# Kernel optimization log

Measured on AMD Instinct MI355X. Metric: run time of the kernel, lower is better.

The kernel has to match this reference:

```python
import jax, jax.numpy as jnp
import numpy as np

K = 3
STRIDE = 1
PAD = 1
DIL = 1


def _unfold(a):
    # a: (N, C, H, W) -> patches (N, C, K*K, oH, oW), matching torch.F.unfold
    # channel-major ordering (c slowest, then kernel row, then kernel col).
    N, C, H, W = a.shape
    oH = (H + 2 * PAD - DIL * (K - 1) - 1) // STRIDE + 1
    oW = (W + 2 * PAD - DIL * (K - 1) - 1) // STRIDE + 1
    ap = jnp.pad(a, ((0, 0), (0, 0), (PAD, PAD), (PAD, PAD)))
    cols = []
    for i in range(K):
        for j in range(K):
            cols.append(ap[:, :,
                           i * DIL: i * DIL + (oH - 1) * STRIDE + 1: STRIDE,
                           j * DIL: j * DIL + (oW - 1) * STRIDE + 1: STRIDE])
    return jnp.stack(cols, axis=2)  # (N, C, K*K, oH, oW)


def setup_inputs() -> dict:
    key = jax.random.key(0)
    k1, k2, k3, k4, k5 = jax.random.split(key, 5)
    N, C, O, H, W = 4, 128, 256, 128, 128
    x = jax.random.normal(k1, (N, C, H, W), dtype=jnp.float32)
    depth = jax.random.uniform(k2, (N, 1, H, W), dtype=jnp.float32)
    camera_params = jax.random.normal(k3, (N, 4), dtype=jnp.float32)
    weight = jax.random.normal(k4, (O, C, K, K), dtype=jnp.float32) * 0.05
    bias = jax.random.normal(k5, (O,), dtype=jnp.float32) * 0.05
    return {"x": x, "depth": depth, "camera_params": camera_params,
            "weight": weight, "bias": bias}


def reference(x, depth, camera_params, weight, bias):
    # camera_params is accepted but unused, mirroring the torch module.
    O, C = weight.shape[0], weight.shape[1]
    xp = _unfold(x)        # (N, C, kk, oH, oW)
    dp = _unfold(depth)    # (N, 1, kk, oH, oW)
    w = weight.reshape(O, C, K * K)
    # depth-modulated im2col GEMM: sum_{c,p} w[o,c,p] * x_patch * d_patch
    out = jnp.einsum('ocp,ncpxy->noxy', w, xp * dp)
    return out + bias[None, :, None, None]
```

## Files before the change

kernel.cpp:

```cpp
#include <hip/hip_runtime.h>
#include <stdint.h>


#define C_IN 128
#define O_OUT 256
#define HW 128
#define NB 4
#define PADW 130

#define XD_ELEMS ((size_t)NB * PADW * PADW * C_IN)
#define XD_BYTES (XD_ELEMS * 2)
#define WT_ELEMS ((size_t)O_OUT * C_IN * 9)
#define WT_BYTES (WT_ELEMS * 2)

typedef __attribute__((ext_vector_type(8))) short short8;
typedef __attribute__((ext_vector_type(4))) float f32x4;
typedef __attribute__((ext_vector_type(2))) float f32x2;
typedef __attribute__((ext_vector_type(4))) unsigned uint4v;

__device__ __forceinline__ unsigned f2bf_bits(float f) {
  unsigned u = __builtin_bit_cast(unsigned, f);
  return (u + 0x7fffu + ((u >> 16) & 1u)) >> 16;
}

__device__ __forceinline__ void async_load16(const void* g, void* l) {
  __builtin_amdgcn_global_load_lds(
      (__attribute__((address_space(1))) void*)g,
      (__attribute__((address_space(3))) void*)l, 16, 0, 0);
}

__global__ __launch_bounds__(256) void prep_all(const float* __restrict__ x,
                                                const float* __restrict__ depth,
                                                const float* __restrict__ w,
                                                short* __restrict__ xd,
                                                short* __restrict__ wt2) {
  const int R = blockIdx.x;
  const int tid = threadIdx.x;

  if (R >= NB * HW * 2 + NB) {
    int gid = (R - (NB * HW * 2 + NB)) * 4608 + tid;
#pragma unroll
    for (int i = 0; i < 18; ++i, gid += 256) {
      const int j = gid & 7;
      const int lane = (gid >> 3) & 63;
      const int t = (gid >> 9) & 3;
      const int wm = (gid >> 11) & 1;
      const int g2 = gid >> 12;
      const int s = g2 % 36;
      const int o0 = g2 / 36;
      const int ln = lane & 15, q = lane >> 4;
      const int o = (o0 << 7) + (wm << 6) + (t << 4) + ln;
      const int cc = s / 9;
      const int tap = s % 9;
      const int c = (cc << 5) + (q << 3) + j;
      wt2[gid] = (short)f2bf_bits(w[((size_t)o * C_IN + c) * 9 + tap]);
    }
    return;
  }

  if (R >= NB * HW * 2) {
    const int n = R - NB * HW * 2;
    uint4v* base0 = (uint4v*)(xd + (size_t)n * PADW * PADW * C_IN);
    uint4v* base1 = (uint4v*)(xd + ((size_t)n * PADW + (PADW - 1)) * PADW * C_IN);
    const uint4v z = {0u, 0u, 0u, 0u};
    const int per_row = PADW * C_IN * 2 / 16;
    for (int i = tid; i < per_row; i += 256) {
      base0[i] = z;
      base1[i] = z;
    }
    return;
  }

  __shared__ __align__(16) unsigned s32[HW * 36];

  const int n = R >> 8;
  const int y = (R >> 1) & 127;
  const int h = R & 1;
  const int lane = tid & 63;
  const int wave = tid >> 6;

  {
    unsigned* row = (unsigned*)(xd + (size_t)(n * PADW + y + 1) * PADW * C_IN);
    if (tid < 32) row[(h << 5) + tid] = 0u;
    else if (tid < 64) row[(size_t)(PADW - 1) * 64 + (h << 5) + (tid - 32)] = 0u;
  }

  const f32x2 d2 = *(const f32x2*)(depth + ((size_t)n * HW + y) * HW + 2 * lane);
  const float* xrow =
      x + (((size_t)(n * C_IN + (h << 6)) * HW) + y) * HW + 2 * lane;
#pragma unroll
  for (int it = 0; it < 8; ++it) {
    const int cp = (wave << 3) + it;
    const f32x2 va = *(const f32x2*)(xrow + (size_t)(2 * cp) * HW * HW);
    const f32x2 vb = *(const f32x2*)(xrow + (size_t)(2 * cp + 1) * HW * HW);
    s32[(2 * lane) * 36 + cp] =
        f2bf_bits(va.x * d2.x) | (f2bf_bits(vb.x * d2.x) << 16);
    s32[(2 * lane + 1) * 36 + cp] =
        f2bf_bits(va.y * d2.y) | (f2bf_bits(vb.y * d2.y) << 16);
  }
  __syncthreads();

  unsigned* orow = (unsigned*)(xd + ((size_t)(n * PADW + y + 1) * PADW + 1) * C_IN);
#pragma unroll
  for (int i = 0; i < 4; ++i) {
    const int flat = tid + (i << 8);
    const int px = flat >> 3, jj = flat & 7;
    const uint4v v = *(const uint4v*)&s32[px * 36 + (jj << 2)];
    *(uint4v*)&orow[(size_t)px * 64 + (h << 5) + (jj << 2)] = v;
  }
}

__global__ __launch_bounds__(256, 2) void conv_mfma(
    const short* __restrict__ xd, const short* __restrict__ wt2,
    const float* __restrict__ bias, float* __restrict__ out) {
  __shared__ __align__(16) short xbuf[2][16640];

  const int tid = threadIdx.x;
  const int bx = blockIdx.x;
  const int n = bx >> 6;
  const int y = (bx & 63) << 1;
  const int o0b = blockIdx.y;
  const int lane = tid & 63;
  const int wave = tid >> 6;
  const int wm = wave & 1, wn = wave >> 1;
  const int ln = lane & 15, q = lane >> 4;

  const short* wbase = wt2 + (size_t)o0b * 147456 + (wm << 11) + (lane << 3);

  const short* xsrc0 = xd + (size_t)(n * PADW + y) * PADW * C_IN +
                       (tid >> 2) * C_IN + (tid & 3) * 8;

  f32x4 acc[4][8] = {};
  short8 areg[2][4];

  auto loadA = [&](int s, int p) {
#pragma unroll
    for (int t = 0; t < 4; ++t)
      areg[p][t] = *(const short8*)(wbase + (size_t)s * 4096 + t * 512);
  };

  {
    short* xdst = &xbuf[0][0] + tid * 8;
#pragma unroll
    for (int j = 0; j < 8; ++j)
      async_load16(xsrc0 + j * 8192, xdst + j * 2048);
    if (tid < 32) async_load16(xsrc0 + 8 * 8192, xdst + 8 * 2048);
  }
  loadA(0, 0);
  __syncthreads();

#pragma unroll
  for (int cc = 0; cc < 4; ++cc) {
#pragma unroll
    for (int tap = 0; tap < 9; ++tap) {
      const int s = cc * 9 + tap;
      if (s + 1 < 36) loadA(s + 1, (s + 1) & 1);

      if (cc + 1 < 4) {
        const short* sp = xsrc0 + ((cc + 1) << 5);
        short* xdst = &xbuf[(cc + 1) & 1][0] + tid * 8;
        if (tap < 8) async_load16(sp + tap * 8192, xdst + tap * 2048);
        if (tap == 0 && tid < 32)
          async_load16(sp + 8 * 8192, xdst + 8 * 2048);
      }

      const int ti = tap / 3, tj = tap % 3;
      const int rbase = (wn + ti) * 130 + tj;

      short8 b[8];
#pragma unroll
      for (int u = 0; u < 8; ++u)
        b[u] = *(const short8*)(&xbuf[cc & 1][0] +
                                (rbase + (u << 4) + ln) * 32 + (q << 3));
      __builtin_amdgcn_s_setprio(1);
#pragma unroll
      for (int t = 0; t < 4; ++t)
#pragma unroll
        for (int u = 0; u < 8; ++u)
          acc[t][u] = __builtin_amdgcn_mfma_f32_16x16x32_bf16(
              areg[s & 1][t], b[u], acc[t][u], 0, 0, 0);
      __builtin_amdgcn_s_setprio(0);
    }
    if (cc + 1 < 4) __syncthreads();
  }

#pragma unroll
  for (int t = 0; t < 4; ++t) {
    const int ob = (o0b << 7) + (wm << 6) + (t << 4) + (q << 2);
#pragma unroll
    for (int u = 0; u < 8; ++u) {
      const int xcol = (u << 4) + ln;
      const int yrow = y + wn;
#pragma unroll
      for (int r = 0; r < 4; ++r) {
        const int o = ob + r;
        out[(((size_t)n * O_OUT + o) * HW + yrow) * HW + xcol] =
            acc[t][u][r] + bias[o];
      }
    }
  }
}

__global__ void conv_naive(const float* __restrict__ x,
                           const float* __restrict__ depth,
                           const float* __restrict__ w,
                           const float* __restrict__ bias,
                           float* __restrict__ out) {
  const int gid = blockIdx.x * 256 + threadIdx.x;
  if (gid >= NB * O_OUT * HW * HW) return;
  const int xc = gid & 127;
  const int y = (gid >> 7) & 127;
  const int o = (gid >> 14) & 255;
  const int n = gid >> 22;
  float s = bias[o];
  for (int c = 0; c < C_IN; ++c)
    for (int i = 0; i < 3; ++i) {
      const int yy = y + i - 1;
      if (yy < 0 || yy >= HW) continue;
      for (int j = 0; j < 3; ++j) {
        const int xx = xc + j - 1;
        if (xx < 0 || xx >= HW) continue;
        s += w[((o * C_IN + c) * 3 + i) * 3 + j] *
             x[(((size_t)n * C_IN + c) * HW + yy) * HW + xx] *
             depth[((size_t)n * HW + yy) * HW + xx];
      }
    }
  out[gid] = s;
}

extern "C" void kernel_launch(void* const* d_in, const int* in_sizes, int n_in,
                              void* d_out, int out_size, void* d_ws, size_t ws_size,
                              hipStream_t stream) {
  const float* x = (const float*)d_in[0];
  const float* depth = (const float*)d_in[1];
  const float* weight = (const float*)d_in[3];
  const float* bias = (const float*)d_in[4];
  float* out = (float*)d_out;

  const size_t need = XD_BYTES + WT_BYTES;
  if (ws_size < need) {
    conv_naive<<<(NB * O_OUT * HW * HW + 255) / 256, 256, 0, stream>>>(
        x, depth, weight, bias, out);
    return;
  }

  short* xd = (short*)d_ws;
  short* wt2 = (short*)((char*)d_ws + XD_BYTES);

  prep_all<<<NB * HW * 2 + NB + 64, 256, 0, stream>>>(x, depth, weight, xd, wt2);
  conv_mfma<<<dim3(NB * HW / 2, 2), 256, 0, stream>>>(xd, wt2, bias, out);
}
```

Before: 128.4 us.

## Retile conv waves to cover all 128 outputs and half the pixel columns

Each wave in the MFMA conv kernel now computes 128 output channels by 64 pixels instead of 64 channels by 128 pixels. Every wave loads 8 weight fragments from global per step and only 4 activation fragments from LDS, which cuts LDS reads but doubles global/L2 weight traffic per wave and the areg register footprint. The weight prep layout is rewritten to match, and the activation prep now does per-lane scalar loads packed into 16-byte LDS stores instead of 2-wide loads with scattered 4-byte stores. The larger weight register set may put pressure on occupancy at the two-blocks-per-CU launch bound.

```diff
diff --git a/kernel.cpp b/kernel.cpp
--- a/kernel.cpp
+++ b/kernel.cpp
@@ -43,13 +43,12 @@
     for (int i = 0; i < 18; ++i, gid += 256) {
       const int j = gid & 7;
       const int lane = (gid >> 3) & 63;
-      const int t = (gid >> 9) & 3;
-      const int wm = (gid >> 11) & 1;
+      const int T = (gid >> 9) & 7;
       const int g2 = gid >> 12;
       const int s = g2 % 36;
       const int o0 = g2 / 36;
       const int ln = lane & 15, q = lane >> 4;
-      const int o = (o0 << 7) + (wm << 6) + (t << 4) + ln;
+      const int o = (o0 << 7) + (T << 4) + ln;
       const int cc = s / 9;
       const int tap = s % 9;
       const int c = (cc << 5) + (q << 3) + j;
@@ -85,18 +84,26 @@
     else if (tid < 64) row[(size_t)(PADW - 1) * 64 + (h << 5) + (tid - 32)] = 0u;
   }
 
-  const f32x2 d2 = *(const f32x2*)(depth + ((size_t)n * HW + y) * HW + 2 * lane);
-  const float* xrow =
-      x + (((size_t)(n * C_IN + (h << 6)) * HW) + y) * HW + 2 * lane;
-#pragma unroll
-  for (int it = 0; it < 8; ++it) {
-    const int cp = (wave << 3) + it;
-    const f32x2 va = *(const f32x2*)(xrow + (size_t)(2 * cp) * HW * HW);
-    const f32x2 vb = *(const f32x2*)(xrow + (size_t)(2 * cp + 1) * HW * HW);
-    s32[(2 * lane) * 36 + cp] =
-        f2bf_bits(va.x * d2.x) | (f2bf_bits(vb.x * d2.x) << 16);
-    s32[(2 * lane + 1) * 36 + cp] =
-        f2bf_bits(va.y * d2.y) | (f2bf_bits(vb.y * d2.y) << 16);
+  const float d0 = depth[((size_t)n * HW + y) * HW + lane];
+  const float d1 = depth[((size_t)n * HW + y) * HW + 64 + lane];
+  const float* xbase = x + (((size_t)(n * C_IN + (h << 6)) * HW) + y) * HW;
+#pragma unroll
+  for (int gg = 0; gg < 2; ++gg) {
+    const int g = (wave << 1) + gg;
+    const float* xc = xbase + ((size_t)(g << 3)) * HW * HW;
+#pragma unroll
+    for (int ph = 0; ph < 2; ++ph) {
+      const int px = (ph << 6) + lane;
+      const float d = ph ? d1 : d0;
+      uint4v v;
+#pragma unroll
+      for (int k = 0; k < 4; ++k) {
+        const float a = xc[(size_t)(2 * k) * HW * HW + px];
+        const float b2 = xc[(size_t)(2 * k + 1) * HW * HW + px];
+        v[k] = f2bf_bits(a * d) | (f2bf_bits(b2 * d) << 16);
+      }
+      *(uint4v*)&s32[px * 36 + (g << 2)] = v;
+    }
   }
   __syncthreads();
 
@@ -122,20 +129,21 @@
   const int o0b = blockIdx.y;
   const int lane = tid & 63;
   const int wave = tid >> 6;
-  const int wm = wave & 1, wn = wave >> 1;
+  const int wn = wave & 1;
+  const int wp = wave >> 1;
   const int ln = lane & 15, q = lane >> 4;
 
-  const short* wbase = wt2 + (size_t)o0b * 147456 + (wm << 11) + (lane << 3);
+  const short* wbase = wt2 + (size_t)o0b * 147456 + (lane << 3);
 
   const short* xsrc0 = xd + (size_t)(n * PADW + y) * PADW * C_IN +
                        (tid >> 2) * C_IN + (tid & 3) * 8;
 
-  f32x4 acc[4][8] = {};
-  short8 areg[2][4];
+  f32x4 acc[8][4] = {};
+  short8 areg[2][8];
 
   auto loadA = [&](int s, int p) {
 #pragma unroll
-    for (int t = 0; t < 4; ++t)
+    for (int t = 0; t < 8; ++t)
       areg[p][t] = *(const short8*)(wbase + (size_t)s * 4096 + t * 512);
   };
 
@@ -165,18 +173,18 @@
       }
 
       const int ti = tap / 3, tj = tap % 3;
-      const int rbase = (wn + ti) * 130 + tj;
-
-      short8 b[8];
-#pragma unroll
-      for (int u = 0; u < 8; ++u)
+      const int rbase = (wn + ti) * 130 + tj + (wp << 6);
+
+      short8 b[4];
+#pragma unroll
+      for (int u = 0; u < 4; ++u)
         b[u] = *(const short8*)(&xbuf[cc & 1][0] +
                                 (rbase + (u << 4) + ln) * 32 + (q << 3));
       __builtin_amdgcn_s_setprio(1);
 #pragma unroll
-      for (int t = 0; t < 4; ++t)
-#pragma unroll
-        for (int u = 0; u < 8; ++u)
+      for (int t = 0; t < 8; ++t)
+#pragma unroll
+        for (int u = 0; u < 4; ++u)
           acc[t][u] = __builtin_amdgcn_mfma_f32_16x16x32_bf16(
               areg[s & 1][t], b[u], acc[t][u], 0, 0, 0);
       __builtin_amdgcn_s_setprio(0);
@@ -184,13 +192,13 @@
     if (cc + 1 < 4) __syncthreads();
   }
 
-#pragma unroll
-  for (int t = 0; t < 4; ++t) {
-    const int ob = (o0b << 7) + (wm << 6) + (t << 4) + (q << 2);
-#pragma unroll
-    for (int u = 0; u < 8; ++u) {
-      const int xcol = (u << 4) + ln;
-      const int yrow = y + wn;
+  const int yrow = y + wn;
+#pragma unroll
+  for (int t = 0; t < 8; ++t) {
+    const int ob = (o0b << 7) + (t << 4) + (q << 2);
+#pragma unroll
+    for (int u = 0; u < 4; ++u) {
+      const int xcol = (wp << 6) + (u << 4) + ln;
 #pragma unroll
       for (int r = 0; r < 4; ++r) {
         const int o = ob + r;
```

Result: slower. 137.6 us (+7.2%).

## Prefetch B fragments into registers, XOR-swizzle LDS layout, remap block order

Applied to the files above, without the earlier changes.

The B operand is now double-buffered in registers, so each tap reads the next tap's fragments from LDS while the MFMAs for the current tap run. The 16-byte chunks within each pixel's 32-channel LDS slot are XOR-swizzled to cut bank conflicts on the strided reads. The 2D grid is flattened into a swizzled 1D block index that interleaves output-channel halves and spreads row blocks across XCDs to improve L2 locality. The extra breg array raises register pressure, which may hurt occupancy under launch_bounds(256,2).

```diff
diff --git a/kernel.cpp b/kernel.cpp
--- a/kernel.cpp
+++ b/kernel.cpp
@@ -116,10 +116,11 @@
   __shared__ __align__(16) short xbuf[2][16640];
 
   const int tid = threadIdx.x;
-  const int bx = blockIdx.x;
+  const int swz = ((blockIdx.x & 7) << 6) + (blockIdx.x >> 3);
+  const int o0b = swz & 1;
+  const int bx = swz >> 1;
   const int n = bx >> 6;
   const int y = (bx & 63) << 1;
-  const int o0b = blockIdx.y;
   const int lane = tid & 63;
   const int wave = tid >> 6;
   const int wm = wave & 1, wn = wave >> 1;
@@ -128,16 +129,26 @@
   const short* wbase = wt2 + (size_t)o0b * 147456 + (wm << 11) + (lane << 3);
 
   const short* xsrc0 = xd + (size_t)(n * PADW + y) * PADW * C_IN +
-                       (tid >> 2) * C_IN + (tid & 3) * 8;
+                       (tid >> 2) * C_IN + ((tid & 3) ^ ((tid >> 3) & 3)) * 8;
 
   f32x4 acc[4][8] = {};
   short8 areg[2][4];
+  short8 breg[2][8];
 
   auto loadA = [&](int s, int p) {
 #pragma unroll
     for (int t = 0; t < 4; ++t)
       areg[p][t] = *(const short8*)(wbase + (size_t)s * 4096 + t * 512);
   };
+  auto readB = [&](int buf, int ti, int tj, int p) {
+    const int rbase = (wn + ti) * 130 + tj;
+#pragma unroll
+    for (int u = 0; u < 8; ++u) {
+      const int px = rbase + (u << 4) + ln;
+      const int qx = (q ^ ((px >> 1) & 3)) << 3;
+      breg[p][u] = *(const short8*)(&xbuf[buf][0] + px * 32 + qx);
+    }
+  };
 
   {
     short* xdst = &xbuf[0][0] + tid * 8;
@@ -148,6 +159,7 @@
   }
   loadA(0, 0);
   __syncthreads();
+  readB(0, 0, 0, 0);
 
 #pragma unroll
   for (int cc = 0; cc < 4; ++cc) {
@@ -164,33 +176,30 @@
           async_load16(sp + 8 * 8192, xdst + 8 * 2048);
       }
 
-      const int ti = tap / 3, tj = tap % 3;
-      const int rbase = (wn + ti) * 130 + tj;
-
-      short8 b[8];
-#pragma unroll
-      for (int u = 0; u < 8; ++u)
-        b[u] = *(const short8*)(&xbuf[cc & 1][0] +
-                                (rbase + (u << 4) + ln) * 32 + (q << 3));
+      if (tap < 8) readB(cc & 1, (tap + 1) / 3, (tap + 1) % 3, (tap + 1) & 1);
+
       __builtin_amdgcn_s_setprio(1);
 #pragma unroll
       for (int t = 0; t < 4; ++t)
 #pragma unroll
         for (int u = 0; u < 8; ++u)
           acc[t][u] = __builtin_amdgcn_mfma_f32_16x16x32_bf16(
-              areg[s & 1][t], b[u], acc[t][u], 0, 0, 0);
+              areg[s & 1][t], breg[tap & 1][u], acc[t][u], 0, 0, 0);
       __builtin_amdgcn_s_setprio(0);
     }
-    if (cc + 1 < 4) __syncthreads();
-  }
-
+    if (cc + 1 < 4) {
+      __syncthreads();
+      readB((cc + 1) & 1, 0, 0, 0);
+    }
+  }
+
+  const int yrow = y + wn;
 #pragma unroll
   for (int t = 0; t < 4; ++t) {
     const int ob = (o0b << 7) + (wm << 6) + (t << 4) + (q << 2);
 #pragma unroll
     for (int u = 0; u < 8; ++u) {
       const int xcol = (u << 4) + ln;
-      const int yrow = y + wn;
 #pragma unroll
       for (int r = 0; r < 4; ++r) {
         const int o = ob + r;
@@ -248,5 +257,5 @@
   short* wt2 = (short*)((char*)d_ws + XD_BYTES);
 
   prep_all<<<NB * HW * 2 + NB + 64, 256, 0, stream>>>(x, depth, weight, xd, wt2);
-  conv_mfma<<<dim3(NB * HW / 2, 2), 256, 0, stream>>>(xd, wt2, bias, out);
-}
+  conv_mfma<<<dim3(NB * HW), 256, 0, stream>>>(xd, wt2, bias, out);
+}
```

Result: slower. 161.1 us (+25.5%).
